# Kernel optimization log

Hardware: AMD Instinct MI355X
Metric: run time of the kernel (lower is better)

## Reference

```python
import jax, jax.numpy as jnp
import numpy as np
from jax import lax

TAU = 0.1
DT = 0.001
UNITS = 1024
B, T = 16, 2048


def setup_inputs() -> dict:
    key = jax.random.key(0)
    inputs = jax.random.normal(key, (B, T, UNITS), dtype=jnp.float32)
    level_var = jnp.zeros((1, UNITS), dtype=jnp.float32)
    e = np.exp(-DT / TAU)
    smoothing_init = np.log(e / (1.0 - e)).astype(np.float32)
    smoothing_var = jnp.ones((1, UNITS), dtype=jnp.float32) * smoothing_init
    return {"inputs": inputs, "level_var": level_var, "smoothing_var": smoothing_var}


def reference(inputs, level_var, smoothing_var):
    # inputs: [B, T, U]; level_var, smoothing_var: [1, U]
    s = jax.nn.sigmoid(smoothing_var)  # [1, U]
    level0 = jnp.broadcast_to(level_var, (inputs.shape[0], inputs.shape[2]))  # [B, U]

    def step(level, x_t):
        new = (1.0 - s) * x_t + s * level  # [B, U]
        return new, new

    _, levels = lax.scan(step, level0, jnp.swapaxes(inputs, 0, 1))  # [T, B, U]
    return jnp.swapaxes(levels, 0, 1)  # [B, T, U]
```

## Files before the change

kernel.cpp:

```cpp
#include <hip/hip_runtime.h>


constexpr int B  = 16;
constexpr int T  = 2048;
constexpr int U  = 1024;
constexpr int C  = 8;
constexpr int L  = T / C;
constexpr int D1 = 32;
constexpr int D2 = 16;
constexpr int BU = B * U;

__device__ __forceinline__ float sigmoidf(float x) {
    return 1.0f / (1.0f + __expf(-x));
}

__global__ __launch_bounds__(64, 2) void lowpass_partial(
    const float* __restrict__ in,
    const float* __restrict__ smooth,
    float* __restrict__ P)
{
    const int lane = threadIdx.x;
    const int blk  = blockIdx.x;
    const int c    = blk >> 8;
    const int r    = blk & 255;
    const int b    = r >> 4;
    const int u    = ((r & 15) << 6) + lane;

    const float s   = sigmoidf(smooth[u]);
    const float oms = 1.0f - s;

    const float* __restrict__ ip = in + (size_t)b * T * U + (size_t)(c * L) * U + u;

    float lv = 0.0f;
    float buf[D1];
    #pragma unroll
    for (int i = 0; i < D1; ++i) buf[i] = ip[(size_t)i * U];

    int t = 0;
    for (; t < L - D1; t += D1) {
        #pragma unroll
        for (int j = 0; j < D1; ++j) {
            float x = buf[j];
            buf[j] = ip[(size_t)(t + D1 + j) * U];
            lv = fmaf(s, lv, oms * x);
        }
    }
    #pragma unroll
    for (int j = 0; j < D1; ++j) {
        lv = fmaf(s, lv, oms * buf[j]);
    }

    P[(size_t)c * BU + (size_t)b * U + u] = lv;
}

__global__ __launch_bounds__(64, 2) void lowpass_scan(
    const float* __restrict__ in,
    const float* __restrict__ level0,
    const float* __restrict__ smooth,
    const float* __restrict__ P,
    float* __restrict__ out)
{
    const int lane = threadIdx.x;
    const int blk  = blockIdx.x;
    const int c    = blk >> 8;
    const int r    = blk & 255;
    const int b    = r >> 4;
    const int u    = ((r & 15) << 6) + lane;
    const int chain = b * U + u;

    const float s   = sigmoidf(smooth[u]);
    const float oms = 1.0f - s;

    float sL = s;
    #pragma unroll
    for (int i = 0; i < 8; ++i) sL *= sL;

    float lv = level0[u];
    for (int i = 0; i < c; ++i) {
        lv = fmaf(sL, lv, P[(size_t)i * BU + chain]);
    }

    const size_t base = (size_t)b * T * U + (size_t)(c * L) * U + u;
    const float* __restrict__ ip = in  + base;
    float*       __restrict__ op = out + base;

    float buf[D2];
    #pragma unroll
    for (int i = 0; i < D2; ++i) buf[i] = ip[(size_t)i * U];

    int t = 0;
    for (; t < L - D2; t += D2) {
        #pragma unroll
        for (int j = 0; j < D2; ++j) {
            float x = buf[j];
            buf[j] = ip[(size_t)(t + D2 + j) * U];
            lv = fmaf(s, lv, oms * x);
            op[(size_t)(t + j) * U] = lv;
        }
    }
    #pragma unroll
    for (int j = 0; j < D2; ++j) {
        lv = fmaf(s, lv, oms * buf[j]);
        op[(size_t)(t + j) * U] = lv;
    }
}

extern "C" void kernel_launch(void* const* d_in, const int* in_sizes, int n_in,
                              void* d_out, int out_size, void* d_ws, size_t ws_size,
                              hipStream_t stream) {
    const float* in     = (const float*)d_in[0];
    const float* level0 = (const float*)d_in[1];
    const float* smooth = (const float*)d_in[2];
    float* out          = (float*)d_out;
    float* P            = (float*)d_ws;

    dim3 block(64);
    dim3 grid(C * (BU / 64));

    hipLaunchKernelGGL(lowpass_partial, grid, block, 0, stream, in, smooth, P);
    hipLaunchKernelGGL(lowpass_scan,    grid, block, 0, stream, in, level0, smooth, P, out);
}
```

Measured before the change: 254.2 us.

## Vectorize scan to float4 per thread, double chunk count, nontemporal stores

Each thread now handles four adjacent units with 128-bit loads and stores instead of one float, so there are fewer memory instructions per byte moved. When the workspace allows, the time axis is split into 16 chunks instead of 8, which restores parallelism lost to the wider per-thread work. Output stores use nontemporal hints to avoid polluting the cache. Prefetch depths are reduced to limit register pressure, at the cost of fewer loads in flight per thread.

After: 256.0 us. Within noise of the previous version (+0.7%).

```diff
diff --git a/kernel.cpp b/kernel.cpp
--- a/kernel.cpp
+++ b/kernel.cpp
@@ -1,122 +1,166 @@
 #include <hip/hip_runtime.h>
 
 
-constexpr int B  = 16;
-constexpr int T  = 2048;
-constexpr int U  = 1024;
-constexpr int C  = 8;
-constexpr int L  = T / C;
-constexpr int D1 = 32;
-constexpr int D2 = 16;
-constexpr int BU = B * U;
+typedef float f32x4 __attribute__((ext_vector_type(4)));
+
+constexpr int B   = 16;
+constexpr int T   = 2048;
+constexpr int U   = 1024;
+constexpr int U4  = U / 4;
+constexpr int BU4 = B * U4;
 
 __device__ __forceinline__ float sigmoidf(float x) {
     return 1.0f / (1.0f + __expf(-x));
 }
 
-__global__ __launch_bounds__(64, 2) void lowpass_partial(
-    const float* __restrict__ in,
+template <int C>
+__global__ __launch_bounds__(64) void lowpass_partial(
+    const f32x4* __restrict__ in,
     const float* __restrict__ smooth,
-    float* __restrict__ P)
+    f32x4*       __restrict__ P)
 {
-    const int lane = threadIdx.x;
-    const int blk  = blockIdx.x;
-    const int c    = blk >> 8;
-    const int r    = blk & 255;
-    const int b    = r >> 4;
-    const int u    = ((r & 15) << 6) + lane;
+    constexpr int L  = T / C;
+    constexpr int D1 = 16;
+    static_assert(L > D1 && L % D1 == 0, "prefetch");
 
-    const float s   = sigmoidf(smooth[u]);
-    const float oms = 1.0f - s;
+    const int tid = blockIdx.x * 64 + (int)threadIdx.x;
+    const int c   = tid >> 12;
+    const int lg  = tid & (BU4 - 1);
+    const int b   = lg >> 8;
+    const int ug  = lg & (U4 - 1);
 
-    const float* __restrict__ ip = in + (size_t)b * T * U + (size_t)(c * L) * U + u;
+    const f32x4 sm = reinterpret_cast<const f32x4*>(smooth)[ug];
+    const float s0 = sigmoidf(sm.x), s1 = sigmoidf(sm.y),
+                s2 = sigmoidf(sm.z), s3 = sigmoidf(sm.w);
+    const float o0 = 1.0f - s0, o1 = 1.0f - s1,
+                o2 = 1.0f - s2, o3 = 1.0f - s3;
 
-    float lv = 0.0f;
-    float buf[D1];
+    const f32x4* __restrict__ ip = in + (b * T + c * L) * U4 + ug;
+
+    float a0 = 0.0f, a1 = 0.0f, a2 = 0.0f, a3 = 0.0f;
+    f32x4 buf[D1];
     #pragma unroll
-    for (int i = 0; i < D1; ++i) buf[i] = ip[(size_t)i * U];
+    for (int i = 0; i < D1; ++i) buf[i] = ip[i * U4];
 
     int t = 0;
     for (; t < L - D1; t += D1) {
         #pragma unroll
         for (int j = 0; j < D1; ++j) {
-            float x = buf[j];
-            buf[j] = ip[(size_t)(t + D1 + j) * U];
-            lv = fmaf(s, lv, oms * x);
+            f32x4 x = buf[j];
+            buf[j] = ip[(t + D1 + j) * U4];
+            a0 = fmaf(s0, a0, o0 * x.x);
+            a1 = fmaf(s1, a1, o1 * x.y);
+            a2 = fmaf(s2, a2, o2 * x.z);
+            a3 = fmaf(s3, a3, o3 * x.w);
         }
     }
     #pragma unroll
     for (int j = 0; j < D1; ++j) {
-        lv = fmaf(s, lv, oms * buf[j]);
+        f32x4 x = buf[j];
+        a0 = fmaf(s0, a0, o0 * x.x);
+        a1 = fmaf(s1, a1, o1 * x.y);
+        a2 = fmaf(s2, a2, o2 * x.z);
+        a3 = fmaf(s3, a3, o3 * x.w);
+    }
+    f32x4 part; part.x = a0; part.y = a1; part.z = a2; part.w = a3;
+    P[c * BU4 + lg] = part;
+}
+
+template <int C>
+__global__ __launch_bounds__(64) void lowpass_scan(
+    const f32x4* __restrict__ in,
+    const float* __restrict__ level0,
+    const float* __restrict__ smooth,
+    const f32x4* __restrict__ P,
+    f32x4*       __restrict__ out)
+{
+    constexpr int L    = T / C;
+    constexpr int D2   = 8;
+    constexpr int LOG2L = 31 - __builtin_clz(L);
+    static_assert(L > D2 && L % D2 == 0, "prefetch");
+    static_assert((1 << LOG2L) == L, "pow2");
+
+    const int tid = blockIdx.x * 64 + (int)threadIdx.x;
+    const int c   = tid >> 12;
+    const int lg  = tid & (BU4 - 1);
+    const int b   = lg >> 8;
+    const int ug  = lg & (U4 - 1);
+
+    const f32x4 sm = reinterpret_cast<const f32x4*>(smooth)[ug];
+    const float s0 = sigmoidf(sm.x), s1 = sigmoidf(sm.y),
+                s2 = sigmoidf(sm.z), s3 = sigmoidf(sm.w);
+    const float o0 = 1.0f - s0, o1 = 1.0f - s1,
+                o2 = 1.0f - s2, o3 = 1.0f - s3;
+
+    float sL0 = s0, sL1 = s1, sL2 = s2, sL3 = s3;
+    #pragma unroll
+    for (int i = 0; i < LOG2L; ++i) {
+        sL0 *= sL0; sL1 *= sL1; sL2 *= sL2; sL3 *= sL3;
     }
 
-    P[(size_t)c * BU + (size_t)b * U + u] = lv;
-}
-
-__global__ __launch_bounds__(64, 2) void lowpass_scan(
-    const float* __restrict__ in,
-    const float* __restrict__ level0,
-    const float* __restrict__ smooth,
-    const float* __restrict__ P,
-    float* __restrict__ out)
-{
-    const int lane = threadIdx.x;
-    const int blk  = blockIdx.x;
-    const int c    = blk >> 8;
-    const int r    = blk & 255;
-    const int b    = r >> 4;
-    const int u    = ((r & 15) << 6) + lane;
-    const int chain = b * U + u;
-
-    const float s   = sigmoidf(smooth[u]);
-    const float oms = 1.0f - s;
-
-    float sL = s;
-    #pragma unroll
-    for (int i = 0; i < 8; ++i) sL *= sL;
-
-    float lv = level0[u];
+    const f32x4 l0 = reinterpret_cast<const f32x4*>(level0)[ug];
+    float v0 = l0.x, v1 = l0.y, v2 = l0.z, v3 = l0.w;
     for (int i = 0; i < c; ++i) {
-        lv = fmaf(sL, lv, P[(size_t)i * BU + chain]);
+        f32x4 p = P[i * BU4 + lg];
+        v0 = fmaf(sL0, v0, p.x);
+        v1 = fmaf(sL1, v1, p.y);
+        v2 = fmaf(sL2, v2, p.z);
+        v3 = fmaf(sL3, v3, p.w);
     }
 
-    const size_t base = (size_t)b * T * U + (size_t)(c * L) * U + u;
-    const float* __restrict__ ip = in  + base;
-    float*       __restrict__ op = out + base;
+    const int base = (b * T + c * L) * U4 + ug;
+    const f32x4* __restrict__ ip = in  + base;
+    f32x4*       __restrict__ op = out + base;
 
-    float buf[D2];
+    f32x4 buf[D2];
     #pragma unroll
-    for (int i = 0; i < D2; ++i) buf[i] = ip[(size_t)i * U];
+    for (int i = 0; i < D2; ++i) buf[i] = ip[i * U4];
 
     int t = 0;
     for (; t < L - D2; t += D2) {
         #pragma unroll
         for (int j = 0; j < D2; ++j) {
-            float x = buf[j];
-            buf[j] = ip[(size_t)(t + D2 + j) * U];
-            lv = fmaf(s, lv, oms * x);
-            op[(size_t)(t + j) * U] = lv;
+            f32x4 x = buf[j];
+            buf[j] = ip[(t + D2 + j) * U4];
+            v0 = fmaf(s0, v0, o0 * x.x);
+            v1 = fmaf(s1, v1, o1 * x.y);
+            v2 = fmaf(s2, v2, o2 * x.z);
+            v3 = fmaf(s3, v3, o3 * x.w);
+            f32x4 r; r.x = v0; r.y = v1; r.z = v2; r.w = v3;
+            __builtin_nontemporal_store(r, &op[(t + j) * U4]);
         }
     }
     #pragma unroll
     for (int j = 0; j < D2; ++j) {
-        lv = fmaf(s, lv, oms * buf[j]);
-        op[(size_t)(t + j) * U] = lv;
+        f32x4 x = buf[j];
+        v0 = fmaf(s0, v0, o0 * x.x);
+        v1 = fmaf(s1, v1, o1 * x.y);
+        v2 = fmaf(s2, v2, o2 * x.z);
+        v3 = fmaf(s3, v3, o3 * x.w);
+        f32x4 r; r.x = v0; r.y = v1; r.z = v2; r.w = v3;
+        __builtin_nontemporal_store(r, &op[(t + j) * U4]);
     }
 }
 
 extern "C" void kernel_launch(void* const* d_in, const int* in_sizes, int n_in,
                               void* d_out, int out_size, void* d_ws, size_t ws_size,
                               hipStream_t stream) {
-    const float* in     = (const float*)d_in[0];
+    const f32x4* in     = (const f32x4*)d_in[0];
     const float* level0 = (const float*)d_in[1];
     const float* smooth = (const float*)d_in[2];
-    float* out          = (float*)d_out;
-    float* P            = (float*)d_ws;
+    f32x4* out          = (f32x4*)d_out;
+    f32x4* P            = (f32x4*)d_ws;
 
     dim3 block(64);
-    dim3 grid(C * (BU / 64));
-
-    hipLaunchKernelGGL(lowpass_partial, grid, block, 0, stream, in, smooth, P);
-    hipLaunchKernelGGL(lowpass_scan,    grid, block, 0, stream, in, level0, smooth, P, out);
+    if (ws_size >= (size_t)16 * BU4 * sizeof(f32x4)) {
+        constexpr int C = 16;
+        dim3 grid(C * BU4 / 64);
+        hipLaunchKernelGGL(lowpass_partial<C>, grid, block, 0, stream, in, smooth, P);
+        hipLaunchKernelGGL(lowpass_scan<C>,    grid, block, 0, stream, in, level0, smooth, P, out);
+    } else {
+        constexpr int C = 8;
+        dim3 grid(C * BU4 / 64);
+        hipLaunchKernelGGL(lowpass_partial<C>, grid, block, 0, stream, in, smooth, P);
+        hipLaunchKernelGGL(lowpass_scan<C>,    grid, block, 0, stream, in, level0, smooth, P, out);
+    }
 }
```
